# Optimization experiments

Measured on AMD Instinct MI355X. Metric: run time of the kernel, lower is better.

The kernel has to match this reference:

```python
import jax, jax.numpy as jnp
import numpy as np

STRIDE = 2
F_SCALE = 4


def _layer_norm(x, eps=1e-5):
    # F.layer_norm over the last 3 dims (C,H,W), no affine
    m = jnp.mean(x, axis=(1, 2, 3), keepdims=True)
    v = jnp.var(x, axis=(1, 2, 3), keepdims=True)
    return (x - m) * jax.lax.rsqrt(v + eps)


def _conv(x, w, b, dil, pad):
    y = jax.lax.conv_general_dilated(
        x, w, window_strides=(1, 1), padding=[(pad, pad), (pad, pad)],
        rhs_dilation=(dil, dil), dimension_numbers=('NCHW', 'OIHW', 'NCHW'))
    return y + b[None, :, None, None]


def _unshuffle(x, f):
    # [B,C,H,W] -> [B*f*f, C, H/f, W/f]; sub-image k=dy*f+dx samples offsets (dy,dx) stride f
    B, C, H, W = x.shape
    sh, sw = H // f, W // f
    x = x.reshape(B, C, sh, f, sw, f)
    x = x.transpose(0, 3, 5, 1, 2, 4)  # [B, dy, dx, C, sh, sw]
    return x.reshape(B * f * f, C, sh, sw)


def _shuffle(x, B, f):
    # inverse of _unshuffle: [B*f*f, C, sh, sw] -> [B, C, sh*f, sw*f]
    _, C, sh, sw = x.shape
    x = x.reshape(B, f, f, C, sh, sw)
    x = x.transpose(0, 3, 4, 1, 5, 2)  # [B, C, sh, dy, sw, dx]
    return x.reshape(B, C, sh * f, sw * f)


def _attention(x, wqk, f):
    B, C, H, W = x.shape
    E = wqk.shape[1]
    ph, pw = (-H) % f, (-W) % f
    xx = _layer_norm(x)
    if ph or pw:
        xx = jnp.pad(xx, ((0, 0), (0, 0), (0, ph), (0, pw)))
        xp = jnp.pad(x, ((0, 0), (0, 0), (0, ph), (0, pw)))
    else:
        xp = x
    sub = _unshuffle(xx, f)   # [Bf, C, sh, sw]
    v = _unshuffle(xp, f)     # [Bf, C, sh, sw]
    Bf, _, sh, sw = sub.shape
    N = sh * sw
    q = sub.transpose(0, 2, 3, 1).reshape(Bf, N, C)
    vf = v.transpose(0, 2, 3, 1).reshape(Bf, N, C)
    qk = jnp.einsum('bnc,ce->bne', q, wqk)
    qk = qk / (jnp.linalg.norm(qk, axis=-1, keepdims=True) + 1e-8)
    attn = (jnp.einsum('bne,bme->bnm', qk, qk) + 1.0) / np.sqrt(E).astype(np.float32)
    attn = jax.nn.softmax(attn, axis=-1)
    out = jnp.einsum('bnm,bmc->bnc', attn, vf)
    out = out.reshape(Bf, sh, sw, C).transpose(0, 3, 1, 2)
    out = _shuffle(out, B, f)
    return out[:, :, :H, :W]


def setup_inputs() -> dict:
    key = jax.random.key(0)
    ks = jax.random.split(key, 8)
    B, C, H, W = 2, 128, 192, 192
    E = C  # ss_exp_factor = 1.0
    x = jax.random.normal(ks[0], (B, C, H, W), jnp.float32)
    lim = 1.414 * np.sqrt(6.0 / (C + E))  # xavier_uniform, gain=1.414
    wqk = jax.random.uniform(ks[1], (C, E), jnp.float32, -lim, lim)
    s = np.sqrt(2.0 / (C * 9)).astype(np.float32)
    w1 = jax.random.normal(ks[2], (C, C, 3, 3), jnp.float32) * s
    b1 = jnp.zeros((C,), jnp.float32)
    w2 = jax.random.normal(ks[3], (C, C, 3, 3), jnp.float32) * s
    b2 = jnp.zeros((C,), jnp.float32)
    w3 = jax.random.normal(ks[4], (C, C, 1, 1), jnp.float32) * np.sqrt(2.0 / C).astype(np.float32)
    b3 = jnp.zeros((C,), jnp.float32)
    return {"x": x, "wqk": wqk, "w1": w1, "b1": b1, "w2": w2, "b2": b2, "w3": w3, "b3": b3}


def reference(x, wqk, w1, b1, w2, b2, w3, b3):
    f = F_SCALE * STRIDE
    y = x + _attention(x, wqk, f)
    h = jax.nn.relu(_conv(y, w1, b1, STRIDE, STRIDE))
    h = jax.nn.relu(_conv(h, w2, b2, STRIDE, STRIDE))
    h = _conv(h, w3, b3, 1, 0)
    return x + h
```

## Files before the change

### kernel.cpp

```cpp
#include <hip/hip_runtime.h>
#include <math.h>

#define CCH 128
#define HH 192
#define WW 192
#define BB 2
#define HW (HH*WW)
#define CHW (CCH*HW)
#define BF 128
#define NN 576
#define SH 24

typedef __attribute__((ext_vector_type(8))) short short8;
typedef __attribute__((ext_vector_type(4))) float floatx4;
typedef unsigned int uint32;
typedef unsigned short ushort;

__device__ __forceinline__ unsigned short bf16r(float f) {
    uint32 u = __float_as_uint(f);
    u += 0x7fffu + ((u >> 16) & 1u);
    return (unsigned short)(u >> 16);
}

__global__ __launch_bounds__(256) void k_reduce(const float* __restrict__ x, float* __restrict__ stats) {
    int b = blockIdx.y;
    const float4* p = (const float4*)(x + (size_t)b*CHW) + (size_t)blockIdx.x*4096;
    float s = 0.f, sq = 0.f;
#pragma unroll
    for (int k = 0; k < 16; ++k) {
        float4 v = p[threadIdx.x + 256*k];
        s  += v.x + v.y + v.z + v.w;
        sq += v.x*v.x + v.y*v.y + v.z*v.z + v.w*v.w;
    }
    for (int off = 32; off; off >>= 1) { s += __shfl_down(s, off); sq += __shfl_down(sq, off); }
    __shared__ float ls[4], lq[4];
    int wave = threadIdx.x >> 6, lane = threadIdx.x & 63;
    if (lane == 0) { ls[wave] = s; lq[wave] = sq; }
    __syncthreads();
    if (threadIdx.x == 0) {
        atomicAdd(&stats[2*b],   ls[0]+ls[1]+ls[2]+ls[3]);
        atomicAdd(&stats[2*b+1], lq[0]+lq[1]+lq[2]+lq[3]);
    }
}

__global__ void k_finalize(float* stats) {
    int b = threadIdx.x;
    if (b < BB) {
        float s = stats[2*b], sq = stats[2*b+1];
        float mean = s / (float)CHW;
        float var = sq / (float)CHW - mean*mean;
        stats[4 + 2*b] = mean;
        stats[5 + 2*b] = rsqrtf(var + 1e-5f);
    }
}

__global__ __launch_bounds__(256) void k_unshuffle(const float* __restrict__ x, const float* __restrict__ stats,
                                                   ushort* __restrict__ Vt, ushort* __restrict__ Xnb) {
    __shared__ float t[128][65];
    int x0 = blockIdx.x * 64;
    int y  = blockIdx.y;
    int b  = blockIdx.z;
    float mean = stats[4+2*b], istd = stats[5+2*b];
    const float* src = x + (size_t)b*CHW + (size_t)y*WW + x0;
#pragma unroll
    for (int k = 0; k < 32; ++k) {
        int idx = threadIdx.x + 256*k;
        int c = idx >> 6, xl = idx & 63;
        t[c][xl] = src[(size_t)c*HW + xl];
    }
    __syncthreads();
    int i = y >> 3, dy = y & 7;
#pragma unroll
    for (int k = 0; k < 32; ++k) {
        int idx = threadIdx.x + 256*k;
        int xl = idx & 63, c = idx >> 6;
        int xx = x0 + xl;
        int j = xx >> 3, dx = xx & 7;
        int bf = (b << 6) + (dy << 3) + dx;
        int n = i*SH + j;
        Vt[((size_t)bf*CCH + c)*NN + n] = bf16r(t[c][xl]);
    }
#pragma unroll
    for (int k = 0; k < 16; ++k) {
        int idx = threadIdx.x + 256*k;
        int c2 = idx & 63, xl = idx >> 6;
        int c = c2 * 2;
        int xx = x0 + xl;
        int j = xx >> 3, dx = xx & 7;
        int bf = (b << 6) + (dy << 3) + dx;
        int n = i*SH + j;
        float v0 = (t[c][xl]   - mean) * istd;
        float v1 = (t[c+1][xl] - mean) * istd;
        uint32 p = (uint32)bf16r(v0) | ((uint32)bf16r(v1) << 16);
        *(uint32*)&Xnb[((size_t)bf*NN + n)*CCH + c] = p;
    }
}

__global__ __launch_bounds__(256) void k_qk(const ushort* __restrict__ Xnb, const ushort* __restrict__ wqkTb,
                                            ushort* __restrict__ qkn) {
    __shared__ ushort As[64*136];
    __shared__ ushort Bs[128*136];
    int bid = blockIdx.x;
    int bf = bid / 9, tile = bid % 9;
    int n0 = tile * 64;
    int tid = threadIdx.x;
    int wv = tid >> 6, l = tid & 63, quad = l >> 4, l15 = l & 15;
    {
        const uint4* asrc = (const uint4*)(Xnb + ((size_t)bf*NN + n0)*CCH);
        const uint4* bsrc = (const uint4*)wqkTb;
#pragma unroll
        for (int k = 0; k < 4; ++k) {
            int idx = tid + 256*k;
            int row = idx >> 4, co = idx & 15;
            *(uint4*)&As[row*136 + co*8] = asrc[idx];
        }
#pragma unroll
        for (int k = 0; k < 8; ++k) {
            int idx = tid + 256*k;
            int row = idx >> 4, co = idx & 15;
            *(uint4*)&Bs[row*136 + co*8] = bsrc[idx];
        }
    }
    __syncthreads();
    int qb = wv*16;
    short8 a[4];
#pragma unroll
    for (int kk = 0; kk < 4; ++kk)
        a[kk] = *(const short8*)&As[(qb + l15)*136 + kk*32 + quad*8];
    floatx4 acc[8];
#pragma unroll
    for (int nt = 0; nt < 8; ++nt) acc[nt] = (floatx4){0.f,0.f,0.f,0.f};
#pragma unroll
    for (int kk = 0; kk < 4; ++kk)
#pragma unroll
        for (int nt = 0; nt < 8; ++nt) {
            const short8 bfr = *(const short8*)&Bs[(nt*16 + l15)*136 + kk*32 + quad*8];
            acc[nt] = __builtin_amdgcn_mfma_f32_16x16x32_bf16(a[kk], bfr, acc[nt], 0, 0, 0);
        }
    float ss[4] = {0.f,0.f,0.f,0.f};
#pragma unroll
    for (int nt = 0; nt < 8; ++nt)
#pragma unroll
        for (int r = 0; r < 4; ++r) ss[r] += acc[nt][r]*acc[nt][r];
#pragma unroll
    for (int off = 1; off < 16; off <<= 1)
#pragma unroll
        for (int r = 0; r < 4; ++r) ss[r] += __shfl_xor(ss[r], off);
    float fr[4];
#pragma unroll
    for (int r = 0; r < 4; ++r) fr[r] = 1.f / (sqrtf(ss[r]) + 1e-8f);
    __syncthreads();
    ushort* mys = &As[qb*128];
#pragma unroll
    for (int nt = 0; nt < 8; ++nt)
#pragma unroll
        for (int r = 0; r < 4; ++r)
            mys[(quad*4 + r)*128 + nt*16 + l15] = bf16r(acc[nt][r]*fr[r]);
    uint4* dst = (uint4*)(qkn + ((size_t)bf*NN + n0 + qb)*CCH);
    const uint4* ls = (const uint4*)mys;
#pragma unroll
    for (int k = 0; k < 4; ++k)
        dst[l + 64*k] = ls[l + 64*k];
}

__global__ __launch_bounds__(256, 2) void k_attn(const ushort* __restrict__ qkn, const ushort* __restrict__ Vt_g,
                                                 float* __restrict__ O) {
    __shared__ ushort Qs[64*136];
    __shared__ ushort Ks[64*136];
    __shared__ ushort Vs[128*72];
    __shared__ ushort Ps[64*72];
    int tile = blockIdx.x, bf = blockIdx.y;
    int n0 = tile*64;
    int tid = threadIdx.x;
    int wv = tid >> 6, l = tid & 63, quad = l >> 4, l15 = l & 15;
    int qb = wv*16;

    {
        const uint4* qsrc = (const uint4*)(qkn + ((size_t)bf*NN + n0)*CCH);
#pragma unroll
        for (int k = 0; k < 4; ++k) {
            int idx = tid + 256*k;
            int row = idx >> 4, co = idx & 15;
            *(uint4*)&Qs[row*136 + co*8] = qsrc[idx];
        }
    }

    floatx4 oacc[8];
#pragma unroll
    for (int ct = 0; ct < 8; ++ct) oacc[ct] = (floatx4){0.f,0.f,0.f,0.f};
    float rsum[4] = {0.f,0.f,0.f,0.f};
    const float scale = 0.08838834764831845f;

    for (int mt = 0; mt < 9; ++mt) {
        int m0 = mt*64;
        __syncthreads();
        {
            const uint4* ksrc = (const uint4*)(qkn + ((size_t)bf*NN + m0)*CCH);
#pragma unroll
            for (int k = 0; k < 4; ++k) {
                int idx = tid + 256*k;
                int row = idx >> 4, co = idx & 15;
                *(uint4*)&Ks[row*136 + co*8] = ksrc[idx];
            }
            const uint4* vsrc = (const uint4*)(Vt_g + (size_t)bf*CCH*NN);
            int mo8 = m0 >> 3;
#pragma unroll
            for (int k = 0; k < 4; ++k) {
                int idx = tid + 256*k;
                int c = idx >> 3, ko = idx & 7;
                *(uint4*)&Vs[c*72 + ko*8] = vsrc[(size_t)c*72 + mo8 + ko];
            }
        }
        __syncthreads();

        short8 aq[4];
#pragma unroll
        for (int kk = 0; kk < 4; ++kk)
            aq[kk] = *(const short8*)&Qs[(qb + l15)*136 + kk*32 + quad*8];
        floatx4 sc[4];
#pragma unroll
        for (int t = 0; t < 4; ++t) sc[t] = (floatx4){0.f,0.f,0.f,0.f};
#pragma unroll
        for (int kk = 0; kk < 4; ++kk)
#pragma unroll
            for (int t = 0; t < 4; ++t) {
                const short8 bk = *(const short8*)&Ks[(t*16 + l15)*136 + kk*32 + quad*8];
                sc[t] = __builtin_amdgcn_mfma_f32_16x16x32_bf16(aq[kk], bk, sc[t], 0, 0, 0);
            }

        float pr[4] = {0.f,0.f,0.f,0.f};
#pragma unroll
        for (int t = 0; t < 4; ++t)
#pragma unroll
            for (int r = 0; r < 4; ++r) {
                float p = __expf((sc[t][r] + 1.f)*scale);
                Ps[(qb + quad*4 + r)*72 + t*16 + l15] = bf16r(p);
                pr[r] += p;
            }
#pragma unroll
        for (int off = 1; off < 16; off <<= 1)
#pragma unroll
            for (int r = 0; r < 4; ++r) pr[r] += __shfl_xor(pr[r], off);
#pragma unroll
        for (int r = 0; r < 4; ++r) rsum[r] += pr[r];

        short8 ap[2];
        ap[0] = *(const short8*)&Ps[(qb + l15)*72 + quad*8];
        ap[1] = *(const short8*)&Ps[(qb + l15)*72 + 32 + quad*8];
#pragma unroll
        for (int ct = 0; ct < 8; ++ct)
#pragma unroll
            for (int kk2 = 0; kk2 < 2; ++kk2) {
                const short8 bv = *(const short8*)&Vs[(ct*16 + l15)*72 + kk2*32 + quad*8];
                oacc[ct] = __builtin_amdgcn_mfma_f32_16x16x32_bf16(ap[kk2], bv, oacc[ct], 0, 0, 0);
            }
    }

    float rinv[4];
#pragma unroll
    for (int r = 0; r < 4; ++r) rinv[r] = 1.f / rsum[r];
#pragma unroll
    for (int ct = 0; ct < 8; ++ct)
#pragma unroll
        for (int r = 0; r < 4; ++r)
            O[((size_t)bf*NN + n0 + qb + quad*4 + r)*CCH + ct*16 + l15] = oacc[ct][r]*rinv[r];
}

__global__ __launch_bounds__(256) void k_shuffle_add(const float* __restrict__ O, const float* __restrict__ x,
                                                     uint4* __restrict__ yb) {
    __shared__ float t[128][65];
    int x0 = blockIdx.x * 64;
    int yy = blockIdx.y;
    int b  = blockIdx.z;
    if (blockIdx.x == 0 && threadIdx.x < 64) {
        int oct = threadIdx.x >> 2, p = threadIdx.x & 3;
        int col = (p < 2) ? p : 192 + p;
        uint4 z; z.x = 0; z.y = 0; z.z = 0; z.w = 0;
        yb[((size_t)(b*192 + yy)*16 + oct)*196 + col] = z;
    }
    int i = yy >> 3, dy = yy & 7;
#pragma unroll
    for (int k = 0; k < 32; ++k) {
        int idx = threadIdx.x + 256*k;
        int c = idx & 127, xl = idx >> 7;
        int xx = x0 + xl;
        int j = xx >> 3, dx = xx & 7;
        int bf = (b << 6) + (dy << 3) + dx;
        int n = i*SH + j;
        t[c][xl] = O[((size_t)bf*NN + n)*CCH + c];
    }
    __syncthreads();
    size_t base = (size_t)b*CHW + (size_t)yy*WW + x0;
#pragma unroll
    for (int k = 0; k < 32; ++k) {
        int idx = threadIdx.x + 256*k;
        int c = idx >> 6, xl = idx & 63;
        t[c][xl] += x[base + (size_t)c*HW + xl];
    }
    __syncthreads();
#pragma unroll
    for (int k = 0; k < 4; ++k) {
        int idx = threadIdx.x + 256*k;
        int xl = idx & 63, oc = idx >> 6;
        uint32 d[4];
#pragma unroll
        for (int j = 0; j < 4; ++j) {
            float f0 = t[oc*8 + 2*j][xl];
            float f1 = t[oc*8 + 2*j + 1][xl];
            d[j] = (uint32)bf16r(f0) | ((uint32)bf16r(f1) << 16);
        }
        uint4 v; v.x = d[0]; v.y = d[1]; v.z = d[2]; v.w = d[3];
        yb[((size_t)(b*192 + yy)*16 + oc)*196 + (x0 + xl + 2)] = v;
    }
}

__global__ __launch_bounds__(256) void k_cast_w(const float* __restrict__ w1, const float* __restrict__ w2,
                                                const float* __restrict__ w3, const float* __restrict__ wqk,
                                                uint4* __restrict__ wb1, uint4* __restrict__ wb2,
                                                uint4* __restrict__ w3b, uint4* __restrict__ wqkTb) {
    int id = blockIdx.x*256 + threadIdx.x;
    if (blockIdx.y == 2) {
        if (id < 2048) {
            int co = id >> 4, oct = id & 15;
            uint32 r[4];
#pragma unroll
            for (int j = 0; j < 4; ++j) {
                float f0 = w3[(size_t)co*128 + oct*8 + 2*j];
                float f1 = w3[(size_t)co*128 + oct*8 + 2*j + 1];
                r[j] = (uint32)bf16r(f0) | ((uint32)bf16r(f1) << 16);
            }
            uint4 v; v.x = r[0]; v.y = r[1]; v.z = r[2]; v.w = r[3];
            w3b[id] = v;
            int e = co;
            uint32 r2[4];
#pragma unroll
            for (int j = 0; j < 4; ++j) {
                float f0 = wqk[(size_t)(oct*8 + 2*j)*128 + e];
                float f1 = wqk[(size_t)(oct*8 + 2*j + 1)*128 + e];
                r2[j] = (uint32)bf16r(f0) | ((uint32)bf16r(f1) << 16);
            }
            uint4 v2; v2.x = r2[0]; v2.y = r2[1]; v2.z = r2[2]; v2.w = r2[3];
            wqkTb[id] = v2;
        }
        return;
    }
    const float* w = (blockIdx.y == 0) ? w1 : w2;
    uint4* wb = (blockIdx.y == 0) ? wb1 : wb2;
    int co = id & 127;
    int oct = (id >> 7) & 3;
    int chunk = (id >> 9) & 3;
    int tap = id >> 11;
    int ci0 = chunk*32 + oct*8;
    uint32 r[4];
#pragma unroll
    for (int j = 0; j < 4; ++j) {
        float f0 = w[(size_t)(co*128 + ci0 + 2*j)*9 + tap];
        float f1 = w[(size_t)(co*128 + ci0 + 2*j + 1)*9 + tap];
        r[j] = (uint32)bf16r(f0) | ((uint32)bf16r(f1) << 16);
    }
    uint4 v; v.x = r[0]; v.y = r[1]; v.z = r[2]; v.w = r[3];
    wb[((size_t)(tap*4 + chunk)*4 + oct)*128 + co] = v;
}

__global__ __launch_bounds__(256, 3) void k_conv3m(const uint4* __restrict__ yb, const uint4* __restrict__ wb,
                                                   const float* __restrict__ bias, void* __restrict__ outp,
                                                   int mode) {
    __shared__ uint4 As[864];
    __shared__ uint4 Ws[2][512];
    int xt = blockIdx.x;
    int rg = blockIdx.y;
    int b  = blockIdx.z;
    int par = rg & 1, g = rg >> 1;
    int y0 = 8*g + par;
    int x0 = xt*32;
    int tid = threadIdx.x;
    int wv = tid >> 6, l = tid & 63, quad = l >> 4, l15 = l & 15;
    int yw = y0 + 2*wv;

    if (mode == 0 && xt == 0) {
        int rowp = y0 + 2*(tid >> 6);
        int oct = (tid >> 2) & 15, p = tid & 3;
        int col = (p < 2) ? p : 192 + p;
        uint4 z; z.x = 0; z.y = 0; z.z = 0; z.w = 0;
        ((uint4*)outp)[((size_t)(b*192 + rowp)*16 + oct)*196 + col] = z;
    }

    floatx4 acc[2][8];
#pragma unroll
    for (int mt = 0; mt < 2; ++mt)
#pragma unroll
        for (int nt = 0; nt < 8; ++nt) acc[mt][nt] = (floatx4){0.f,0.f,0.f,0.f};

    const uint4* ybb = yb + (size_t)b*602112;

    for (int chunk = 0; chunk < 4; ++chunk) {
        __syncthreads();
#pragma unroll
        for (int k = 0; k < 4; ++k) {
            int idx = tid + 256*k;
            if (idx < 864) {
                int r = idx / 144;
                int rem = idx - r*144;
                int oct = rem / 36;
                int px = rem - oct*36;
                int grow = y0 - 2 + 2*r;
                uint4 v; v.x = 0; v.y = 0; v.z = 0; v.w = 0;
                if (grow >= 0 && grow < 192)
                    v = ybb[((size_t)grow*16 + chunk*4 + oct)*196 + x0 + px];
                As[idx] = v;
            }
        }
        {
            const uint4* src = wb + (size_t)chunk*512;
            Ws[0][tid]     = src[tid];
            Ws[0][tid+256] = src[tid+256];
        }
        __syncthreads();
#pragma unroll
        for (int tap = 0; tap < 9; ++tap) {
            if (tap < 8) {
                const uint4* src = wb + (size_t)((tap+1)*4 + chunk)*512;
                Ws[(tap+1)&1][tid]     = src[tid];
                Ws[(tap+1)&1][tid+256] = src[tid+256];
            }
            const int ky = tap/3, kx = tap - 3*(tap/3);
            int r = wv + ky;
            const short8 a0 = *(const short8*)&As[(r*4 + quad)*36 + l15 + 2*kx];
            const short8 a1 = *(const short8*)&As[(r*4 + quad)*36 + 16 + l15 + 2*kx];
            const uint4* wbuf = &Ws[tap&1][0];
#pragma unroll
            for (int nt = 0; nt < 8; ++nt) {
                const short8 bf = *(const short8*)&wbuf[quad*128 + nt*16 + l15];
                acc[0][nt] = __builtin_amdgcn_mfma_f32_16x16x32_bf16(a0, bf, acc[0][nt], 0, 0, 0);
                acc[1][nt] = __builtin_amdgcn_mfma_f32_16x16x32_bf16(a1, bf, acc[1][nt], 0, 0, 0);
            }
            __syncthreads();
        }
    }

    if (mode == 0) {
        unsigned short* outb = (unsigned short*)outp;
#pragma unroll
        for (int nt = 0; nt < 8; ++nt) {
            int co = nt*16 + l15;
            float bv = bias[co];
            size_t base = (((size_t)(b*192 + yw)*16 + ((co>>5)*4 + ((co>>3)&3)))*196)*8 + (size_t)(co&7);
#pragma unroll
            for (int mt = 0; mt < 2; ++mt)
#pragma unroll
                for (int rr = 0; rr < 4; ++rr) {
                    int xx = x0 + mt*16 + quad*4 + rr;
                    float v = fmaxf(acc[mt][nt][rr] + bv, 0.f);
                    outb[base + (size_t)(xx+2)*8] = bf16r(v);
                }
        }
    } else {
        unsigned short* outb = (unsigned short*)outp;
#pragma unroll
        for (int nt = 0; nt < 8; ++nt) {
            int co = nt*16 + l15;
            float bv = bias[co];
#pragma unroll
            for (int mt = 0; mt < 2; ++mt)
#pragma unroll
                for (int rr = 0; rr < 4; ++rr) {
                    int xx = x0 + mt*16 + quad*4 + rr;
                    float v = fmaxf(acc[mt][nt][rr] + bv, 0.f);
                    outb[((size_t)b*36864 + (size_t)yw*192 + xx)*128 + co] = bf16r(v);
                }
        }
    }
}

__global__ __launch_bounds__(256, 2) void k_conv1x1m(const ushort* __restrict__ h2b, const uint4* __restrict__ w3b,
                                                     const float* __restrict__ b3, const float* __restrict__ x,
                                                     float* __restrict__ out) {
    __shared__ ushort Hs[128*136];
    __shared__ ushort Ws3[128*136];
    int px0 = blockIdx.x * 128;
    int b = blockIdx.y;
    int tid = threadIdx.x;
    int wv = tid >> 6, l = tid & 63, quad = l >> 4, l15 = l & 15;

    {
        const uint4* hsrc = (const uint4*)(h2b + ((size_t)b*36864 + px0)*128);
#pragma unroll
        for (int k = 0; k < 8; ++k) {
            int idx = tid + 256*k;
            int row = idx >> 4, co8 = idx & 15;
            *(uint4*)&Hs[row*136 + co8*8] = hsrc[idx];
            *(uint4*)&Ws3[row*136 + co8*8] = w3b[idx];
        }
    }
    __syncthreads();

    floatx4 oacc[2][8];
#pragma unroll
    for (int mt = 0; mt < 2; ++mt)
#pragma unroll
        for (int nt = 0; nt < 8; ++nt) oacc[mt][nt] = (floatx4){0.f,0.f,0.f,0.f};

#pragma unroll
    for (int kk = 0; kk < 4; ++kk) {
        const short8 aq0 = *(const short8*)&Hs[(wv*32 + l15)*136 + kk*32 + quad*8];
        const short8 aq1 = *(const short8*)&Hs[(wv*32 + 16 + l15)*136 + kk*32 + quad*8];
#pragma unroll
        for (int nt = 0; nt < 8; ++nt) {
            const short8 bw = *(const short8*)&Ws3[(nt*16 + l15)*136 + kk*32 + quad*8];
            oacc[0][nt] = __builtin_amdgcn_mfma_f32_16x16x32_bf16(aq0, bw, oacc[0][nt], 0, 0, 0);
            oacc[1][nt] = __builtin_amdgcn_mfma_f32_16x16x32_bf16(aq1, bw, oacc[1][nt], 0, 0, 0);
        }
    }

#pragma unroll
    for (int nt = 0; nt < 8; ++nt) {
        int co = nt*16 + l15;
        float bv = b3[co];
        size_t pbase = ((size_t)b*128 + co)*HW + px0 + wv*32 + quad*4;
#pragma unroll
        for (int mt = 0; mt < 2; ++mt) {
            const float4 xv = *(const float4*)&x[pbase + mt*16];
            float4 o;
            o.x = oacc[mt][nt][0] + bv + xv.x;
            o.y = oacc[mt][nt][1] + bv + xv.y;
            o.z = oacc[mt][nt][2] + bv + xv.z;
            o.w = oacc[mt][nt][3] + bv + xv.w;
            *(float4*)&out[pbase + mt*16] = o;
        }
    }
}

extern "C" void kernel_launch(void* const* d_in, const int* in_sizes, int n_in,
                              void* d_out, int out_size, void* d_ws, size_t ws_size,
                              hipStream_t stream) {
    (void)in_sizes; (void)n_in; (void)out_size; (void)ws_size;
    const float* x   = (const float*)d_in[0];
    const float* wqk = (const float*)d_in[1];
    const float* w1  = (const float*)d_in[2];
    const float* b1  = (const float*)d_in[3];
    const float* w2  = (const float*)d_in[4];
    const float* b2  = (const float*)d_in[5];
    const float* w3  = (const float*)d_in[6];
    const float* b3  = (const float*)d_in[7];
    float* out = (float*)d_out;
    char* ws = (char*)d_ws;
    float* stats = (float*)ws;
    const size_t SZ = (size_t)BF * NN * CCH * sizeof(float);
    char* Abase = ws + 256;
    char* Bbase = ws + 256 + SZ;
    char* Cbase = ws + 256 + 2*SZ;
    ushort* Vt  = (ushort*)Abase;
    ushort* Xnb = (ushort*)Bbase;
    ushort* qkn = (ushort*)Cbase;
    float*  O   = (float*)Bbase;
    uint4*  yb  = (uint4*)Cbase;
    uint4*  h1b = (uint4*)Abase;
    ushort* h2b = (ushort*)Bbase;
    uint4* wb1   = (uint4*)(Abase + 20*1024*1024);
    uint4* wb2   = (uint4*)(Abase + 21*1024*1024);
    uint4* w3b   = (uint4*)(Abase + 22*1024*1024);
    uint4* wqkTb = (uint4*)(Abase + 23*1024*1024);

    hipMemsetAsync(stats, 0, 4*sizeof(float), stream);
    k_reduce     <<<dim3(288, 2),     256, 0, stream>>>(x, stats);
    k_finalize   <<<1, 64,            0, stream>>>(stats);
    k_cast_w     <<<dim3(72, 3),      256, 0, stream>>>(w1, w2, w3, wqk, wb1, wb2, w3b, wqkTb);
    k_unshuffle  <<<dim3(3, 192, 2),  256, 0, stream>>>(x, stats, Vt, Xnb);
    k_qk         <<<1152,             256, 0, stream>>>(Xnb, (const ushort*)wqkTb, qkn);
    k_attn       <<<dim3(9, 128),     256, 0, stream>>>(qkn, Vt, O);
    k_shuffle_add<<<dim3(3, 192, 2),  256, 0, stream>>>(O, x, yb);
    k_conv3m     <<<dim3(6, 48, 2),   256, 0, stream>>>(yb,  wb1, b1, (void*)h1b, 0);
    k_conv3m     <<<dim3(6, 48, 2),   256, 0, stream>>>(h1b, wb2, b2, (void*)h2b, 1);
    k_conv1x1m   <<<dim3(288, 2),     256, 0, stream>>>(h2b, w3b, b3, x, out);
}
```

Baseline: 315.8 us.

## Prefetch K/V tiles into registers and alias Q/P LDS in attention kernel

```diff
diff --git a/kernel.cpp b/kernel.cpp
--- a/kernel.cpp
+++ b/kernel.cpp
@@ -163,63 +163,79 @@
         dst[l + 64*k] = ls[l + 64*k];
 }
 
-__global__ __launch_bounds__(256, 2) void k_attn(const ushort* __restrict__ qkn, const ushort* __restrict__ Vt_g,
+__global__ __launch_bounds__(256, 3) void k_attn(const ushort* __restrict__ qkn, const ushort* __restrict__ Vt_g,
                                                  float* __restrict__ O) {
-    __shared__ ushort Qs[64*136];
+    __shared__ ushort QPs[64*136];
     __shared__ ushort Ks[64*136];
     __shared__ ushort Vs[128*72];
-    __shared__ ushort Ps[64*72];
-    int tile = blockIdx.x, bf = blockIdx.y;
+    int id = blockIdx.x;
+    int bfl = id & 7, widx = id >> 3;
+    int tile = widx % 9;
+    int bf = ((widx / 9) << 3) | bfl;
     int n0 = tile*64;
     int tid = threadIdx.x;
     int wv = tid >> 6, l = tid & 63, quad = l >> 4, l15 = l & 15;
     int qb = wv*16;
 
+    const uint4* ksrc_base = (const uint4*)(qkn + (size_t)bf*NN*CCH);
+    const uint4* vsrc = (const uint4*)(Vt_g + (size_t)bf*CCH*NN);
+    uint4 kreg[4], vreg[4];
+
+#pragma unroll
+    for (int k = 0; k < 4; ++k) kreg[k] = ksrc_base[tid + 256*k];
+#pragma unroll
+    for (int k = 0; k < 4; ++k) {
+        int idx = tid + 256*k;
+        vreg[k] = vsrc[(size_t)(idx >> 3)*72 + (idx & 7)];
+    }
+
     {
-        const uint4* qsrc = (const uint4*)(qkn + ((size_t)bf*NN + n0)*CCH);
+        const uint4* qsrc = ksrc_base + (size_t)tile*1024;
 #pragma unroll
         for (int k = 0; k < 4; ++k) {
             int idx = tid + 256*k;
-            int row = idx >> 4, co = idx & 15;
-            *(uint4*)&Qs[row*136 + co*8] = qsrc[idx];
-        }
-    }
+            *(uint4*)&QPs[(idx >> 4)*136 + (idx & 15)*8] = qsrc[idx];
+        }
+    }
+    __syncthreads();
+
+    short8 aq[4];
+#pragma unroll
+    for (int kk = 0; kk < 4; ++kk)
+        aq[kk] = *(const short8*)&QPs[(qb + l15)*136 + kk*32 + quad*8];
 
     floatx4 oacc[8];
 #pragma unroll
     for (int ct = 0; ct < 8; ++ct) oacc[ct] = (floatx4){0.f,0.f,0.f,0.f};
     float rsum[4] = {0.f,0.f,0.f,0.f};
     const float scale = 0.08838834764831845f;
+    ushort* Ps = QPs;
 
     for (int mt = 0; mt < 9; ++mt) {
-        int m0 = mt*64;
         __syncthreads();
-        {
-            const uint4* ksrc = (const uint4*)(qkn + ((size_t)bf*NN + m0)*CCH);
+#pragma unroll
+        for (int k = 0; k < 4; ++k) {
+            int idx = tid + 256*k;
+            *(uint4*)&Ks[(idx >> 4)*136 + (idx & 15)*8] = kreg[k];
+            *(uint4*)&Vs[(idx >> 3)*72 + (idx & 7)*8] = vreg[k];
+        }
+        __syncthreads();
+        if (mt < 8) {
+            const uint4* ks = ksrc_base + (size_t)(mt+1)*1024;
+            int mo8 = ((mt+1)*64) >> 3;
+#pragma unroll
+            for (int k = 0; k < 4; ++k) kreg[k] = ks[tid + 256*k];
 #pragma unroll
             for (int k = 0; k < 4; ++k) {
                 int idx = tid + 256*k;
-                int row = idx >> 4, co = idx & 15;
-                *(uint4*)&Ks[row*136 + co*8] = ksrc[idx];
-            }
-            const uint4* vsrc = (const uint4*)(Vt_g + (size_t)bf*CCH*NN);
-            int mo8 = m0 >> 3;
-#pragma unroll
-            for (int k = 0; k < 4; ++k) {
-                int idx = tid + 256*k;
-                int c = idx >> 3, ko = idx & 7;
-                *(uint4*)&Vs[c*72 + ko*8] = vsrc[(size_t)c*72 + mo8 + ko];
-            }
-        }
-        __syncthreads();
-
-        short8 aq[4];
-#pragma unroll
-        for (int kk = 0; kk < 4; ++kk)
-            aq[kk] = *(const short8*)&Qs[(qb + l15)*136 + kk*32 + quad*8];
+                vreg[k] = vsrc[(size_t)(idx >> 3)*72 + mo8 + (idx & 7)];
+            }
+        }
+
         floatx4 sc[4];
 #pragma unroll
         for (int t = 0; t < 4; ++t) sc[t] = (floatx4){0.f,0.f,0.f,0.f};
+        __builtin_amdgcn_s_setprio(1);
 #pragma unroll
         for (int kk = 0; kk < 4; ++kk)
 #pragma unroll
@@ -227,6 +243,7 @@
                 const short8 bk = *(const short8*)&Ks[(t*16 + l15)*136 + kk*32 + quad*8];
                 sc[t] = __builtin_amdgcn_mfma_f32_16x16x32_bf16(aq[kk], bk, sc[t], 0, 0, 0);
             }
+        __builtin_amdgcn_s_setprio(0);
 
         float pr[4] = {0.f,0.f,0.f,0.f};
 #pragma unroll
@@ -247,6 +264,7 @@
         short8 ap[2];
         ap[0] = *(const short8*)&Ps[(qb + l15)*72 + quad*8];
         ap[1] = *(const short8*)&Ps[(qb + l15)*72 + 32 + quad*8];
+        __builtin_amdgcn_s_setprio(1);
 #pragma unroll
         for (int ct = 0; ct < 8; ++ct)
 #pragma unroll
@@ -254,6 +272,7 @@
                 const short8 bv = *(const short8*)&Vs[(ct*16 + l15)*72 + kk2*32 + quad*8];
                 oacc[ct] = __builtin_amdgcn_mfma_f32_16x16x32_bf16(ap[kk2], bv, oacc[ct], 0, 0, 0);
             }
+        __builtin_amdgcn_s_setprio(0);
     }
 
     float rinv[4];
@@ -567,7 +586,7 @@
     k_cast_w     <<<dim3(72, 3),      256, 0, stream>>>(w1, w2, w3, wqk, wb1, wb2, w3b, wqkTb);
     k_unshuffle  <<<dim3(3, 192, 2),  256, 0, stream>>>(x, stats, Vt, Xnb);
     k_qk         <<<1152,             256, 0, stream>>>(Xnb, (const ushort*)wqkTb, qkn);
-    k_attn       <<<dim3(9, 128),     256, 0, stream>>>(qkn, Vt, O);
+    k_attn       <<<1152,             256, 0, stream>>>(qkn, Vt, O);
     k_shuffle_add<<<dim3(3, 192, 2),  256, 0, stream>>>(O, x, yb);
     k_conv3m     <<<dim3(6, 48, 2),   256, 0, stream>>>(yb,  wb1, b1, (void*)h1b, 0);
     k_conv3m     <<<dim3(6, 48, 2),   256, 0, stream>>>(h1b, wb2, b2, (void*)h2b, 1);
```

Result: slower. 364.2 us (+15.3%).
